# Optimization experiments

Hardware: AMD Instinct MI355X
Metric: run time of the kernel (lower is better)

The kernel has to match this reference:

```python
import jax, jax.numpy as jnp
import numpy as np

KNOTS = 17

def _buffers(dtype=jnp.float32):
    t = jnp.linspace(0.0, 3.0, KNOTS, dtype=dtype)
    dt = 3.0 / (KNOTS - 1)
    w = jnp.full((KNOTS,), 2.0 * dt, dtype=dtype).at[0].set(dt).at[-1].set(dt)
    phi = jnp.exp(-jnp.square(t) / 2.0)
    return t, phi, w * phi


def setup_inputs() -> dict:
    key = jax.random.key(0)
    k1, k2 = jax.random.split(key)
    T, B, D, P = 32, 64, 256, 1024
    proj = jax.random.normal(k1, (T, B, D), dtype=jnp.float32)
    A = jax.random.normal(k2, (D, P), dtype=jnp.float32)
    return {"proj": proj, "A": A}


def reference(proj, A):
    t, phi, weights = _buffers(proj.dtype)
    # column-normalize random projection directions (matches A.div_(norm.clamp_min))
    A = A / jnp.maximum(jnp.linalg.norm(A, axis=0, keepdims=True), 1e-12)
    B = proj.shape[-2]
    # (T, B, P) projections, broadcast against knots -> (T, B, P, K)
    x_t = (proj @ A)[..., None] * t
    # empirical characteristic function averaged over batch dim B (dim -3)
    cos_mean = jnp.cos(x_t).mean(axis=-3)  # (T, P, K)
    sin_mean = jnp.sin(x_t).mean(axis=-3)  # (T, P, K)
    err = jnp.square(cos_mean - phi) + jnp.square(sin_mean)
    statistic = (err @ weights) * B  # (T, P)
    return statistic.mean()
```

## Files before the change

### kernel.cpp

```cpp
#include <hip/hip_runtime.h>

#define T_DIM 32
#define B_DIM 64
#define D_DIM 256
#define P_DIM 1024
#define NK    17
#define DT    0.1875f

#define KC    128
#define LROW  136
#define PROW  264

typedef __bf16 bf16x8 __attribute__((ext_vector_type(8)));
typedef float  f32x16 __attribute__((ext_vector_type(16)));

static __device__ __forceinline__ unsigned short f2bf(float f) {
  unsigned u = __float_as_uint(f);
  u += 0x7fffu + ((u >> 16) & 1u);
  return (unsigned short)(u >> 16);
}

__global__ __launch_bounds__(256) void prep_kernel(const float* __restrict__ proj,
                                                   const float* __restrict__ A,
                                                   unsigned short* __restrict__ projbf,
                                                   unsigned short* __restrict__ ATbf) {
  const int tid = threadIdx.x;
  if (blockIdx.x < 16) {
    __shared__ unsigned short tile[64 * PROW];
    __shared__ float red[4][64];
    __shared__ float invn[64];
    const int pl = tid & 63;
    const int dq = tid >> 6;
    const int p0 = blockIdx.x * 64;
    const float* Ac = A + p0 + pl;
    float s = 0.f;
#pragma unroll 8
    for (int i = 0; i < 64; ++i) {
      float v = Ac[(size_t)(dq * 64 + i) * P_DIM];
      s = fmaf(v, v, s);
    }
    red[dq][pl] = s;
    __syncthreads();
    if (tid < 64) {
      float tot = red[0][pl] + red[1][pl] + red[2][pl] + red[3][pl];
      invn[pl] = rsqrtf(fmaxf(tot, 1e-24f));
    }
    __syncthreads();
    const float inv = invn[pl];
#pragma unroll 8
    for (int i = 0; i < 64; ++i) {
      int d = dq * 64 + i;
      float v = Ac[(size_t)d * P_DIM] * inv;
      tile[pl * PROW + d] = f2bf(v);
    }
    __syncthreads();
#pragma unroll
    for (int r = 0; r < 8; ++r) {
      int idx = tid + r * 256;
      int row = idx >> 5, c = idx & 31;
      uint4 v = *(const uint4*)&tile[row * PROW + c * 8];
      *(uint4*)(ATbf + ((size_t)(p0 + row) * D_DIM + c * 8)) = v;
    }
  } else {
    const int pb = blockIdx.x - 16;
    const float4* src = (const float4*)proj + (size_t)pb * 2048;
    unsigned short* dst = projbf + (size_t)pb * 8192;
#pragma unroll
    for (int r = 0; r < 8; ++r) {
      int i = tid + r * 256;
      float4 v = src[i];
      ushort4 o;
      o.x = f2bf(v.x); o.y = f2bf(v.y); o.z = f2bf(v.z); o.w = f2bf(v.w);
      *(ushort4*)(dst + (size_t)i * 4) = o;
    }
  }
}

__global__ __launch_bounds__(256) void sig_main_kernel(const unsigned short* __restrict__ projbf,
                                                       const unsigned short* __restrict__ ATbf,
                                                       float* __restrict__ partials) {
  __shared__ unsigned short sm[2 * 64 * LROW];
  float* smf = (float*)sm;
  const int tid  = threadIdx.x;
  const int lane = tid & 63;
  const int wv   = tid >> 6;
  const int p0   = blockIdx.x * 64;
  const int t    = blockIdx.y;

  unsigned short* sp = sm;
  unsigned short* sa = sm + 64 * LROW;

  const unsigned short* gp = projbf + (size_t)t * B_DIM * D_DIM;
  const unsigned short* ga = ATbf + (size_t)p0 * D_DIM;

  const int mt = wv >> 1, nt = wv & 1;
  const int mrow = mt * 32 + (lane & 31);
  const int nrow = nt * 32 + (lane & 31);
  const int koff = (lane >> 5) * 8;

  f32x16 acc = {0.f, 0.f, 0.f, 0.f, 0.f, 0.f, 0.f, 0.f,
                0.f, 0.f, 0.f, 0.f, 0.f, 0.f, 0.f, 0.f};

  for (int kc = 0; kc < D_DIM; kc += KC) {
#pragma unroll
    for (int r = 0; r < 4; ++r) {
      int idx = tid + r * 256;
      int row = idx >> 4, c = idx & 15;
      uint4 v = *(const uint4*)(gp + (size_t)row * D_DIM + kc + c * 8);
      *(uint4*)&sp[row * LROW + c * 8] = v;
      uint4 w = *(const uint4*)(ga + (size_t)row * D_DIM + kc + c * 8);
      *(uint4*)&sa[row * LROW + c * 8] = w;
    }
    __syncthreads();

#pragma unroll
    for (int ks = 0; ks < 8; ++ks) {
      int k = ks * 16 + koff;
      bf16x8 af = *(const bf16x8*)&sp[mrow * LROW + k];
      bf16x8 bf = *(const bf16x8*)&sa[nrow * LROW + k];
      acc = __builtin_amdgcn_mfma_f32_32x32x16_bf16(af, bf, acc, 0, 0, 0);
    }
    __syncthreads();
  }

  float cs[NK - 1], ss[NK - 1];
#pragma unroll
  for (int k = 0; k < NK - 1; ++k) { cs[k] = 0.f; ss[k] = 0.f; }
#pragma unroll
  for (int r = 0; r < 16; ++r) {
    float th = acc[r] * DT;
    float s1, c1;
    __sincosf(th, &s1, &c1);
    float twoc = 2.f * c1;
    float ckm1 = 1.f, skm1 = 0.f;
    float ck = c1, sk = s1;
    cs[0] += c1;
    ss[0] += s1;
#pragma unroll
    for (int k = 2; k < NK; ++k) {
      float cn = fmaf(twoc, ck, -ckm1);
      float sn = fmaf(twoc, sk, -skm1);
      cs[k - 1] += cn;
      ss[k - 1] += sn;
      ckm1 = ck; skm1 = sk; ck = cn; sk = sn;
    }
  }

#pragma unroll
  for (int k = 0; k < NK - 1; ++k) {
    cs[k] += __shfl_xor(cs[k], 32, 64);
    ss[k] += __shfl_xor(ss[k], 32, 64);
  }

  if (lane < 32) {
    int p = nt * 32 + (lane & 31);
#pragma unroll
    for (int k = 0; k < NK - 1; ++k) {
      smf[k * 128 + mt * 64 + p]        = cs[k];
      smf[2048 + k * 128 + mt * 64 + p] = ss[k];
    }
  }
  __syncthreads();

  float part = 0.f;
#pragma unroll
  for (int r = 0; r < 4; ++r) {
    int e  = tid + r * 256;
    int k1 = e >> 6;
    int pl = e & 63;
    float C = smf[k1 * 128 + pl] + smf[k1 * 128 + 64 + pl];
    float S = smf[2048 + k1 * 128 + pl] + smf[2048 + k1 * 128 + 64 + pl];
    float cm  = C * (1.f / 64.f);
    float sm_ = S * (1.f / 64.f);
    float tk  = (float)(k1 + 1) * DT;
    float phi = __expf(-0.5f * tk * tk);
    float wk  = ((k1 == NK - 2) ? DT : 2.f * DT) * phi;
    float dc  = cm - phi;
    part = fmaf(wk, fmaf(dc, dc, sm_ * sm_), part);
  }
  part *= (1.f / 512.f);

#pragma unroll
  for (int off = 32; off > 0; off >>= 1)
    part += __shfl_down(part, off, 64);
  __syncthreads();
  if (lane == 0) smf[4096 + wv] = part;
  __syncthreads();
  if (tid == 0)
    partials[blockIdx.y * 16 + blockIdx.x] = smf[4096] + smf[4097] + smf[4098] + smf[4099];
}

__global__ __launch_bounds__(256) void sig_finalize_kernel(const float* __restrict__ partials,
                                                           float* __restrict__ out) {
  __shared__ float red[4];
  const int tid  = threadIdx.x;
  const int lane = tid & 63;
  const int wave = tid >> 6;
  float v = partials[tid] + partials[tid + 256];
#pragma unroll
  for (int off = 32; off > 0; off >>= 1)
    v += __shfl_down(v, off, 64);
  if (lane == 0) red[wave] = v;
  __syncthreads();
  if (tid == 0) out[0] = red[0] + red[1] + red[2] + red[3];
}

extern "C" void kernel_launch(void* const* d_in, const int* in_sizes, int n_in,
                              void* d_out, int out_size, void* d_ws, size_t ws_size,
                              hipStream_t stream) {
  const float* proj = (const float*)d_in[0];
  const float* A    = (const float*)d_in[1];
  float* out        = (float*)d_out;

  unsigned short* projbf = (unsigned short*)d_ws;
  unsigned short* ATbf   = (unsigned short*)((char*)d_ws + 1536u * 1024);
  float* partials        = (float*)((char*)d_ws + 2560u * 1024);

  prep_kernel<<<dim3(80), dim3(256), 0, stream>>>(proj, A, projbf, ATbf);
  sig_main_kernel<<<dim3(16, 32), dim3(256), 0, stream>>>(projbf, ATbf, partials);
  sig_finalize_kernel<<<dim3(1), dim3(256), 0, stream>>>(partials, out);
}
```

Measured before the change: 72.26 us.

## Fuse bf16 conversion, column normalization and final reduction into one kernel

The separate prep and finalize kernels are removed. The main kernel now loads fp32 proj and A directly, converts them to bf16 while staging into LDS, and accumulates column sums of squares of A along the way. Because the projection is linear in each column, the column normalization is applied after the GEMM by scaling the accumulator with 1/norm before the sincos step. Per-block partials are combined with an atomicAdd into an output zeroed by a memset, replacing the finalize launch. In exchange, every t-block redundantly reads fp32 A and recomputes the norms, the global reads are twice as large, and the result now depends on atomic ordering.

```diff
diff --git a/kernel.cpp b/kernel.cpp
--- a/kernel.cpp
+++ b/kernel.cpp
@@ -9,107 +9,86 @@
 
 #define KC    128
 #define LROW  136
-#define PROW  264
 
 typedef __bf16 bf16x8 __attribute__((ext_vector_type(8)));
 typedef float  f32x16 __attribute__((ext_vector_type(16)));
 
-static __device__ __forceinline__ unsigned short f2bf(float f) {
+static __device__ __forceinline__ unsigned f2bf(float f) {
   unsigned u = __float_as_uint(f);
   u += 0x7fffu + ((u >> 16) & 1u);
-  return (unsigned short)(u >> 16);
+  return u >> 16;
 }
 
-__global__ __launch_bounds__(256) void prep_kernel(const float* __restrict__ proj,
-                                                   const float* __restrict__ A,
-                                                   unsigned short* __restrict__ projbf,
-                                                   unsigned short* __restrict__ ATbf) {
-  const int tid = threadIdx.x;
-  if (blockIdx.x < 16) {
-    __shared__ unsigned short tile[64 * PROW];
-    __shared__ float red[4][64];
-    __shared__ float invn[64];
-    const int pl = tid & 63;
-    const int dq = tid >> 6;
-    const int p0 = blockIdx.x * 64;
-    const float* Ac = A + p0 + pl;
-    float s = 0.f;
-#pragma unroll 8
-    for (int i = 0; i < 64; ++i) {
-      float v = Ac[(size_t)(dq * 64 + i) * P_DIM];
-      s = fmaf(v, v, s);
-    }
-    red[dq][pl] = s;
-    __syncthreads();
-    if (tid < 64) {
-      float tot = red[0][pl] + red[1][pl] + red[2][pl] + red[3][pl];
-      invn[pl] = rsqrtf(fmaxf(tot, 1e-24f));
-    }
-    __syncthreads();
-    const float inv = invn[pl];
-#pragma unroll 8
-    for (int i = 0; i < 64; ++i) {
-      int d = dq * 64 + i;
-      float v = Ac[(size_t)d * P_DIM] * inv;
-      tile[pl * PROW + d] = f2bf(v);
-    }
-    __syncthreads();
-#pragma unroll
-    for (int r = 0; r < 8; ++r) {
-      int idx = tid + r * 256;
-      int row = idx >> 5, c = idx & 31;
-      uint4 v = *(const uint4*)&tile[row * PROW + c * 8];
-      *(uint4*)(ATbf + ((size_t)(p0 + row) * D_DIM + c * 8)) = v;
-    }
-  } else {
-    const int pb = blockIdx.x - 16;
-    const float4* src = (const float4*)proj + (size_t)pb * 2048;
-    unsigned short* dst = projbf + (size_t)pb * 8192;
-#pragma unroll
-    for (int r = 0; r < 8; ++r) {
-      int i = tid + r * 256;
-      float4 v = src[i];
-      ushort4 o;
-      o.x = f2bf(v.x); o.y = f2bf(v.y); o.z = f2bf(v.z); o.w = f2bf(v.w);
-      *(ushort4*)(dst + (size_t)i * 4) = o;
-    }
-  }
-}
+__global__ __launch_bounds__(256) void sig_fused_kernel(const float* __restrict__ proj,
+                                                        const float* __restrict__ A,
+                                                        float* __restrict__ out) {
+  __shared__ float smf[9792];
+  unsigned short* sp = (unsigned short*)smf;
+  unsigned short* sa = sp + 64 * LROW;
+  float* normred = smf + 8704;
+  float* invn    = smf + 9728;
 
-__global__ __launch_bounds__(256) void sig_main_kernel(const unsigned short* __restrict__ projbf,
-                                                       const unsigned short* __restrict__ ATbf,
-                                                       float* __restrict__ partials) {
-  __shared__ unsigned short sm[2 * 64 * LROW];
-  float* smf = (float*)sm;
   const int tid  = threadIdx.x;
   const int lane = tid & 63;
   const int wv   = tid >> 6;
   const int p0   = blockIdx.x * 64;
   const int t    = blockIdx.y;
 
-  unsigned short* sp = sm;
-  unsigned short* sa = sm + 64 * LROW;
-
-  const unsigned short* gp = projbf + (size_t)t * B_DIM * D_DIM;
-  const unsigned short* ga = ATbf + (size_t)p0 * D_DIM;
-
   const int mt = wv >> 1, nt = wv & 1;
   const int mrow = mt * 32 + (lane & 31);
   const int nrow = nt * 32 + (lane & 31);
   const int koff = (lane >> 5) * 8;
 
+  const float4* Pg = (const float4*)(proj + (size_t)t * B_DIM * D_DIM);
+  const float4* Ag = (const float4*)(A + p0);
+
+  const int pg = tid & 15;
+  const int dg = tid >> 4;
+
   f32x16 acc = {0.f, 0.f, 0.f, 0.f, 0.f, 0.f, 0.f, 0.f,
                 0.f, 0.f, 0.f, 0.f, 0.f, 0.f, 0.f, 0.f};
+  float nrm[4] = {0.f, 0.f, 0.f, 0.f};
 
   for (int kc = 0; kc < D_DIM; kc += KC) {
 #pragma unroll
     for (int r = 0; r < 4; ++r) {
-      int idx = tid + r * 256;
-      int row = idx >> 4, c = idx & 15;
-      uint4 v = *(const uint4*)(gp + (size_t)row * D_DIM + kc + c * 8);
-      *(uint4*)&sp[row * LROW + c * 8] = v;
-      uint4 w = *(const uint4*)(ga + (size_t)row * D_DIM + kc + c * 8);
-      *(uint4*)&sa[row * LROW + c * 8] = w;
+      int pair = tid + r * 256;
+      int row = pair >> 4, cp = pair & 15;
+      float4 v0 = Pg[row * 64 + kc / 4 + cp * 2];
+      float4 v1 = Pg[row * 64 + kc / 4 + cp * 2 + 1];
+      uint4 w;
+      w.x = f2bf(v0.x) | (f2bf(v0.y) << 16);
+      w.y = f2bf(v0.z) | (f2bf(v0.w) << 16);
+      w.z = f2bf(v1.x) | (f2bf(v1.y) << 16);
+      w.w = f2bf(v1.z) | (f2bf(v1.w) << 16);
+      *(uint4*)&sp[row * LROW + cp * 8] = w;
+    }
+    {
+      float4 va[8];
+#pragma unroll
+      for (int i = 0; i < 8; ++i)
+        va[i] = Ag[(size_t)(kc + dg * 8 + i) * (P_DIM / 4) + pg];
+#pragma unroll
+      for (int j = 0; j < 4; ++j) {
+        float e0 = ((const float*)&va[0])[j], e1 = ((const float*)&va[1])[j];
+        float e2 = ((const float*)&va[2])[j], e3 = ((const float*)&va[3])[j];
+        float e4 = ((const float*)&va[4])[j], e5 = ((const float*)&va[5])[j];
+        float e6 = ((const float*)&va[6])[j], e7 = ((const float*)&va[7])[j];
+        nrm[j] = fmaf(e0, e0, nrm[j]); nrm[j] = fmaf(e1, e1, nrm[j]);
+        nrm[j] = fmaf(e2, e2, nrm[j]); nrm[j] = fmaf(e3, e3, nrm[j]);
+        nrm[j] = fmaf(e4, e4, nrm[j]); nrm[j] = fmaf(e5, e5, nrm[j]);
+        nrm[j] = fmaf(e6, e6, nrm[j]); nrm[j] = fmaf(e7, e7, nrm[j]);
+        uint4 w;
+        w.x = f2bf(e0) | (f2bf(e1) << 16);
+        w.y = f2bf(e2) | (f2bf(e3) << 16);
+        w.z = f2bf(e4) | (f2bf(e5) << 16);
+        w.w = f2bf(e6) | (f2bf(e7) << 16);
+        *(uint4*)&sa[(pg * 4 + j) * LROW + dg * 8] = w;
+      }
+    }
+    if (kc != 0) {
+#pragma unroll
+      for (int j = 0; j < 4; ++j) normred[dg * 64 + pg * 4 + j] = nrm[j];
     }
     __syncthreads();
 
@@ -123,12 +102,21 @@
     __syncthreads();
   }
 
+  if (tid < 64) {
+    float s = 0.f;
+#pragma unroll
+    for (int q = 0; q < 16; ++q) s += normred[q * 64 + tid];
+    invn[tid] = rsqrtf(fmaxf(s, 1e-24f));
+  }
+  __syncthreads();
+  const float invdt = invn[nt * 32 + (lane & 31)] * DT;
+
   float cs[NK - 1], ss[NK - 1];
 #pragma unroll
   for (int k = 0; k < NK - 1; ++k) { cs[k] = 0.f; ss[k] = 0.f; }
 #pragma unroll
   for (int r = 0; r < 16; ++r) {
-    float th = acc[r] * DT;
+    float th = acc[r] * invdt;
     float s1, c1;
     __sincosf(th, &s1, &c1);
     float twoc = 2.f * c1;
@@ -187,22 +175,7 @@
   if (lane == 0) smf[4096 + wv] = part;
   __syncthreads();
   if (tid == 0)
-    partials[blockIdx.y * 16 + blockIdx.x] = smf[4096] + smf[4097] + smf[4098] + smf[4099];
-}
-
-__global__ __launch_bounds__(256) void sig_finalize_kernel(const float* __restrict__ partials,
-                                                           float* __restrict__ out) {
-  __shared__ float red[4];
-  const int tid  = threadIdx.x;
-  const int lane = tid & 63;
-  const int wave = tid >> 6;
-  float v = partials[tid] + partials[tid + 256];
-#pragma unroll
-  for (int off = 32; off > 0; off >>= 1)
-    v += __shfl_down(v, off, 64);
-  if (lane == 0) red[wave] = v;
-  __syncthreads();
-  if (tid == 0) out[0] = red[0] + red[1] + red[2] + red[3];
+    atomicAdd(out, smf[4096] + smf[4097] + smf[4098] + smf[4099]);
 }
 
 extern "C" void kernel_launch(void* const* d_in, const int* in_sizes, int n_in,
@@ -212,11 +185,6 @@
   const float* A    = (const float*)d_in[1];
   float* out        = (float*)d_out;
 
-  unsigned short* projbf = (unsigned short*)d_ws;
-  unsigned short* ATbf   = (unsigned short*)((char*)d_ws + 1536u * 1024);
-  float* partials        = (float*)((char*)d_ws + 2560u * 1024);
-
-  prep_kernel<<<dim3(80), dim3(256), 0, stream>>>(proj, A, projbf, ATbf);
-  sig_main_kernel<<<dim3(16, 32), dim3(256), 0, stream>>>(projbf, ATbf, partials);
-  sig_finalize_kernel<<<dim3(1), dim3(256), 0, stream>>>(partials, out);
+  hipMemsetAsync(out, 0, sizeof(float), stream);
+  sig_fused_kernel<<<dim3(16, 32), dim3(256), 0, stream>>>(proj, A, out);
 }
```

Result: faster. 70.26 us (-2.8%).
